# Optimization experiments

Hardware: AMD Instinct MI355X
Metric: run time of the kernel (lower is better)

The kernel has to match this reference:

```python
import jax, jax.numpy as jnp
import numpy as np

V, E, H = 256, 64, 128  # char vocab, char embedding dim, LSTM hidden per direction
N, L = 16384, 24        # number of words, max chars per word


def _lstm_final(embs_t, mask_t, Wih, Whh, bih, bhh):
    """Masked LSTM scan; returns final hidden state [N, H].
    embs_t: [L, N, E] time-major char embeddings
    mask_t: [L, N, 1] float mask (1 = valid char)
    Gate order matches PyTorch: i, f, g, o.
    """
    Nw = embs_t.shape[1]
    h0 = jnp.zeros((Nw, H), embs_t.dtype)
    c0 = jnp.zeros((Nw, H), embs_t.dtype)

    def step(carry, inp):
        h, c = carry
        x, m = inp
        g = x @ Wih.T + bih + h @ Whh.T + bhh  # [N, 4H]
        i, f, gg, o = jnp.split(g, 4, axis=-1)
        i, f, o = jax.nn.sigmoid(i), jax.nn.sigmoid(f), jax.nn.sigmoid(o)
        gg = jnp.tanh(gg)
        c_new = f * c + i * gg
        h_new = o * jnp.tanh(c_new)
        h = jnp.where(m > 0, h_new, h)
        c = jnp.where(m > 0, c_new, c)
        return (h, c), None

    (hT, _), _ = jax.lax.scan(step, (h0, c0), (embs_t, mask_t))
    return hT


def setup_inputs() -> dict:
    key = jax.random.key(0)
    ks = jax.random.split(key, 12)
    s_ih = 1.0 / np.sqrt(H)
    char_indices = jax.random.randint(ks[0], (N, L), 0, V, dtype=jnp.int64)
    lengths = jax.random.randint(ks[1], (N,), 0, L + 1, dtype=jnp.int32)
    emb_table = jax.random.normal(ks[2], (V, E), jnp.float32) * 0.1
    emb_table = emb_table.at[0].set(0.0)  # padding_idx = 0
    def u(k, shape):
        return jax.random.uniform(k, shape, jnp.float32, -s_ih, s_ih)
    return {
        "char_indices": char_indices,
        "lengths": lengths,
        "emb_table": emb_table,
        "Wih_f": u(ks[3], (4 * H, E)),
        "Whh_f": u(ks[4], (4 * H, H)),
        "bih_f": u(ks[5], (4 * H,)),
        "bhh_f": u(ks[6], (4 * H,)),
        "Wih_b": u(ks[7], (4 * H, E)),
        "Whh_b": u(ks[8], (4 * H, H)),
        "bih_b": u(ks[9], (4 * H,)),
        "bhh_b": u(ks[10], (4 * H,)),
    }


def reference(char_indices, lengths, emb_table, Wih_f, Whh_f, bih_f, bhh_f,
              Wih_b, Whh_b, bih_b, bhh_b):
    # mask of valid char positions per word: [N, L]
    pos = jnp.arange(L)[None, :]
    mask = (pos < lengths[:, None]).astype(jnp.float32)
    embs = emb_table[char_indices] * mask[..., None]  # [N, L, E]

    embs_t = jnp.swapaxes(embs, 0, 1)                 # [L, N, E]
    mask_t = jnp.swapaxes(mask, 0, 1)[..., None]      # [L, N, 1]

    # forward direction: final state = state at last valid step
    h_fwd = _lstm_final(embs_t, mask_t, Wih_f, Whh_f, bih_f, bhh_f)
    # backward direction: flip time; leading pad steps are masked (state stays 0),
    # then valid chars are consumed in reverse -> final state = backward h_n
    h_bwd = _lstm_final(embs_t[::-1], mask_t[::-1], Wih_b, Whh_b, bih_b, bhh_b)

    return jnp.concatenate([h_fwd, h_bwd], axis=-1)   # [N, 2H]
```

## Files before the change

kernel.cpp:

```cpp
#include <hip/hip_runtime.h>
#include <math.h>

#define Vv 256
#define Ee 64
#define Hh 128
#define Nn 16384
#define Ll 24
#define G4 512
#define WB 32
#define NTHR 512
#define NGRP (Nn / WB)
#define NTASK (NGRP * 2)

typedef _Float16 half8 __attribute__((ext_vector_type(8)));
typedef float f32x4 __attribute__((ext_vector_type(4)));

#define KS1 (-1.4426950408889634f)

__global__ void prep_sort_kernel(const float* __restrict__ emb,
                                 const float* __restrict__ Wih_f, const float* __restrict__ Whh_f,
                                 const float* __restrict__ bih_f, const float* __restrict__ bhh_f,
                                 const float* __restrict__ Wih_b, const float* __restrict__ Whh_b,
                                 const float* __restrict__ bih_b, const float* __restrict__ bhh_b,
                                 const int* __restrict__ lens,
                                 _Float16* __restrict__ BP, float* __restrict__ XGq,
                                 int* __restrict__ order) {
  const int tid = threadIdx.x;
  if (blockIdx.x == 1024) {
    __shared__ int hcnt[32];
    __shared__ int hcur[32];
    if (tid < 32) hcnt[tid] = 0;
    __syncthreads();
    for (int i = tid; i < Nn; i += 256) atomicAdd(&hcnt[lens[i]], 1);
    __syncthreads();
    if (tid == 0) {
      int s = 0;
      for (int b = 0; b <= Ll; b++) { hcur[b] = s; s += hcnt[b]; }
    }
    __syncthreads();
    for (int i = tid; i < Nn; i += 256) {
      int p = atomicAdd(&hcur[lens[i]], 1);
      order[p] = i;
    }
    return;
  }
  int i = blockIdx.x * 256 + tid;
  if (i < 2 * Vv * G4) {
    int bank = i & 3, u = (i >> 2) & 127, c = (i >> 9) & 255, d = i >> 17;
    int j = bank * 128 + u;
    const float* Wih = d ? Wih_b : Wih_f;
    const float* bih = d ? bih_b : bih_f;
    const float* bhh = d ? bhh_b : bhh_f;
    float acc = bih[j] + bhh[j];
    const float4* e4 = (const float4*)(emb + c * Ee);
    const float4* w4 = (const float4*)(Wih + j * Ee);
#pragma unroll 4
    for (int k = 0; k < Ee / 4; k++) {
      float4 a = e4[k], b = w4[k];
      acc = fmaf(a.x, b.x, acc); acc = fmaf(a.y, b.y, acc);
      acc = fmaf(a.z, b.z, acc); acc = fmaf(a.w, b.w, acc);
    }
    XGq[i] = (bank == 2) ? acc : acc * KS1;
  }
  if (i < 2 * 4 * 4 * 4 * 128 * 8) {
    int e = i & 7, u = (i >> 3) & 127, g2 = (i >> 10) & 3,
        bank = (i >> 12) & 3, kt = (i >> 14) & 3, d = (i >> 16) & 1;
    int j = bank * 128 + u;
    int k = kt * 32 + g2 * 8 + e;
    const float* Whh = d ? Whh_b : Whh_f;
    float w = Whh[j * Hh + k];
    BP[i] = (_Float16)((bank == 2) ? w : w * KS1);
  }
}

#define PADE_TANH(X, NUM, DEN)                                                \
    float X##_2 = (X) * (X);                                                  \
    float NUM = (X) * fmaf(X##_2, fmaf(X##_2, 1.0f, 105.0f), 945.0f);         \
    float DEN = fmaf(X##_2, fmaf(X##_2, 15.0f, 420.0f), 945.0f);              \
    NUM = fminf(fmaxf(NUM, -DEN), DEN);

#define GATES(ACC, CS, HR, MT, WLEN)                                          \
  _Pragma("unroll") for (int r = 0; r < 4; r++) {                             \
    float Av = __builtin_amdgcn_exp2f(ACC[0][r]);                             \
    float Bv = __builtin_amdgcn_exp2f(ACC[1][r]);                             \
    float yg = ACC[2][r];                                                     \
    float Ev = __builtin_amdgcn_exp2f(ACC[3][r]);                             \
    float aA = 1.0f + Av, aB = 1.0f + Bv, aE = 1.0f + Ev;                     \
    PADE_TANH(yg, gn, gd)                                                     \
    float R1 = __builtin_amdgcn_rcpf(aA * aB * gd);                           \
    float cn = fmaf(CS[r] * aA, gd, gn * aB) * R1;                            \
    PADE_TANH(cn, tn, td)                                                     \
    float R2 = __builtin_amdgcn_rcpf(td * aE);                                \
    float hn = tn * R2;                                                       \
    if (t < WLEN[r]) {                                                        \
      CS[r] = cn; HR[r] = hn;                                                 \
      hw[(MT)*16 + qg * 4 + r][u] = (_Float16)hn;                             \
    }                                                                         \
  }

#define LOADX(XV, P0, MT, TT)                                                 \
  _Pragma("unroll") for (int r = 0; r < 4; r++) {                             \
    int pos = P0[r] + sgn * (TT);                                             \
    pos = pos < 0 ? 0 : pos;                                                  \
    int c = idx_s[(MT)*16 + qg * 4 + r][pos];                                 \
    XV[r] = xq[(c << 7) + u];                                                 \
  }

__global__ __launch_bounds__(NTHR, 2) void bilstm_main(
    const int* __restrict__ cidx, const int* __restrict__ lens,
    const _Float16* __restrict__ BP, const float* __restrict__ XGq,
    const int* __restrict__ order, float* __restrict__ out) {
  __shared__ __align__(16) _Float16 hs[2][WB][136];
  __shared__ int idx_s[WB][Ll];
  __shared__ int wid_s[WB];
  __shared__ int len_s[WB];

  const int tid = threadIdx.x;
  const int lane = tid & 63;
  const int wv = tid >> 6;
  const int qg = lane >> 4;
  const int li = lane & 15;
  const int u = (wv << 4) + li;

  const int task = NTASK - 1 - (int)blockIdx.x;
  const int g = task >> 1;
  const int d = task & 1;
  const int sgn = d ? -1 : 1;

  if (tid < WB) { int w = order[g * WB + tid]; wid_s[tid] = w; len_s[tid] = lens[w]; }
  __syncthreads();
  for (int i = tid; i < WB * Ll; i += NTHR) {
    int w = i / Ll, p = i - w * Ll;
    idx_s[w][p] = cidx[(size_t)wid_s[w] * Ll + p];
  }
  for (int i = tid; i < 2 * WB * 136; i += NTHR) ((_Float16*)hs)[i] = (_Float16)0.0f;
  __syncthreads();

  const int maxlen = len_s[WB - 1];

  half8 Bf[4][4];
  {
    const _Float16* BPd = BP + (size_t)d * 65536;
#pragma unroll
    for (int kt = 0; kt < 4; kt++)
#pragma unroll
      for (int bank = 0; bank < 4; bank++)
        Bf[kt][bank] = *(const half8*)(BPd + (size_t)((((kt * 4 + bank) * 4 + qg) * 128 + u) << 3));
  }

  const f32x4* xq = (const f32x4*)(XGq + (size_t)d * (Vv * G4));

  int wlen0[4], wlen1[4], p0a[4], p0b[4];
#pragma unroll
  for (int r = 0; r < 4; r++) {
    wlen0[r] = len_s[qg * 4 + r];
    wlen1[r] = len_s[16 + qg * 4 + r];
    p0a[r] = d ? (wlen0[r] - 1) : 0;
    p0b[r] = d ? (wlen1[r] - 1) : 0;
  }
  float cst0[4], cst1[4], hreg0[4], hreg1[4];
#pragma unroll
  for (int r = 0; r < 4; r++) { cst0[r] = 0.0f; cst1[r] = 0.0f; hreg0[r] = 0.0f; hreg1[r] = 0.0f; }

  f32x4 x4a[4], x4b[4];
  if (maxlen > 0) { LOADX(x4a, p0a, 0, 0); LOADX(x4b, p0b, 1, 0); }

  for (int t = 0; t < maxlen; t++) {
    _Float16 (*hw)[136] = hs[t & 1];
    const _Float16 (*hr)[136] = hs[(t ^ 1) & 1];

    f32x4 acc0[4], acc1[4];
#pragma unroll
    for (int bank = 0; bank < 4; bank++)
#pragma unroll
      for (int r = 0; r < 4; r++) {
        acc0[bank][r] = x4a[r][bank];
        acc1[bank][r] = x4b[r][bank];
      }

    if (t > 0) {
      half8 a0[4], a1[4];
#pragma unroll
      for (int kt = 0; kt < 4; kt++) {
        a0[kt] = *(const half8*)&hr[li][kt * 32 + qg * 8];
        a1[kt] = *(const half8*)&hr[16 + li][kt * 32 + qg * 8];
      }
#pragma unroll
      for (int bank = 0; bank < 4; bank++) {
        f32x4 v0 = acc0[bank], v1 = acc1[bank];
#pragma unroll
        for (int kt = 0; kt < 4; kt++) {
          v0 = __builtin_amdgcn_mfma_f32_16x16x32_f16(a0[kt], Bf[kt][bank], v0, 0, 0, 0);
          v1 = __builtin_amdgcn_mfma_f32_16x16x32_f16(a1[kt], Bf[kt][bank], v1, 0, 0, 0);
        }
        acc0[bank] = v0; acc1[bank] = v1;
      }
    }

    if (t + 1 < maxlen) { LOADX(x4a, p0a, 0, t + 1); LOADX(x4b, p0b, 1, t + 1); }

    GATES(acc0, cst0, hreg0, 0, wlen0);
    GATES(acc1, cst1, hreg1, 1, wlen1);

    __syncthreads();
  }

#pragma unroll
  for (int r = 0; r < 4; r++) {
    out[(size_t)wid_s[qg * 4 + r] * (2 * Hh) + d * Hh + u] = hreg0[r];
    out[(size_t)wid_s[16 + qg * 4 + r] * (2 * Hh) + d * Hh + u] = hreg1[r];
  }
}

extern "C" void kernel_launch(void* const* d_in, const int* in_sizes, int n_in,
                              void* d_out, int out_size, void* d_ws, size_t ws_size,
                              hipStream_t stream) {
  const int* cidx = (const int*)d_in[0];
  const int* lens = (const int*)d_in[1];
  const float* emb = (const float*)d_in[2];
  const float* Wih_f = (const float*)d_in[3];
  const float* Whh_f = (const float*)d_in[4];
  const float* bih_f = (const float*)d_in[5];
  const float* bhh_f = (const float*)d_in[6];
  const float* Wih_b = (const float*)d_in[7];
  const float* Whh_b = (const float*)d_in[8];
  const float* bih_b = (const float*)d_in[9];
  const float* bhh_b = (const float*)d_in[10];
  float* out = (float*)d_out;

  char* base = (char*)d_ws;
  _Float16* BP = (_Float16*)base;
  float* XGq = (float*)(base + 262144);
  int* order = (int*)(base + 262144 + 1048576);

  prep_sort_kernel<<<1025, 256, 0, stream>>>(
      emb, Wih_f, Whh_f, bih_f, bhh_f, Wih_b, Whh_b, bih_b, bhh_b, lens, BP, XGq, order);
  bilstm_main<<<NTASK, NTHR, 0, stream>>>(cidx, lens, BP, XGq, order, out);
}
```

Baseline: 147.6 us.

## Halve words per block to 16, raise occupancy, compute sigmoids via Pade tanh

Each block now handles 16 words instead of 32, which halves per-thread state registers and MFMA work per step. Launch bounds go from 2 to 4 blocks per CU, so more blocks can overlap the serial per-timestep latency. The sigmoid gates are rewritten as 0.5*(1+tanh(x/2)) using the rational Pade tanh with folded reciprocals, removing the exp2 calls. The trade-offs are twice as many blocks and reloads of the recurrent weights, fewer independent MFMA chains per wave to hide latency, and the accuracy of the Pade approximation for the sigmoid gates.

```diff
diff --git a/kernel.cpp b/kernel.cpp
--- a/kernel.cpp
+++ b/kernel.cpp
@@ -7,15 +7,13 @@
 #define Nn 16384
 #define Ll 24
 #define G4 512
-#define WB 32
+#define WB 16
 #define NTHR 512
 #define NGRP (Nn / WB)
 #define NTASK (NGRP * 2)
 
 typedef _Float16 half8 __attribute__((ext_vector_type(8)));
 typedef float f32x4 __attribute__((ext_vector_type(4)));
-
-#define KS1 (-1.4426950408889634f)
 
 __global__ void prep_sort_kernel(const float* __restrict__ emb,
                                  const float* __restrict__ Wih_f, const float* __restrict__ Whh_f,
@@ -60,7 +58,7 @@
       acc = fmaf(a.x, b.x, acc); acc = fmaf(a.y, b.y, acc);
       acc = fmaf(a.z, b.z, acc); acc = fmaf(a.w, b.w, acc);
     }
-    XGq[i] = (bank == 2) ? acc : acc * KS1;
+    XGq[i] = (bank == 2) ? acc : acc * 0.5f;
   }
   if (i < 2 * 4 * 4 * 4 * 128 * 8) {
     int e = i & 7, u = (i >> 3) & 127, g2 = (i >> 10) & 3,
@@ -69,7 +67,7 @@
     int k = kt * 32 + g2 * 8 + e;
     const float* Whh = d ? Whh_b : Whh_f;
     float w = Whh[j * Hh + k];
-    BP[i] = (_Float16)((bank == 2) ? w : w * KS1);
+    BP[i] = (_Float16)((bank == 2) ? w : w * 0.5f);
   }
 }
 
@@ -79,34 +77,38 @@
     float DEN = fmaf(X##_2, fmaf(X##_2, 15.0f, 420.0f), 945.0f);              \
     NUM = fminf(fmaxf(NUM, -DEN), DEN);
 
-#define GATES(ACC, CS, HR, MT, WLEN)                                          \
+#define GATES(ACC, CS, HR, WLEN)                                              \
   _Pragma("unroll") for (int r = 0; r < 4; r++) {                             \
-    float Av = __builtin_amdgcn_exp2f(ACC[0][r]);                             \
-    float Bv = __builtin_amdgcn_exp2f(ACC[1][r]);                             \
+    float xi = ACC[0][r];                                                     \
+    float xf = ACC[1][r];                                                     \
     float yg = ACC[2][r];                                                     \
-    float Ev = __builtin_amdgcn_exp2f(ACC[3][r]);                             \
-    float aA = 1.0f + Av, aB = 1.0f + Bv, aE = 1.0f + Ev;                     \
-    PADE_TANH(yg, gn, gd)                                                     \
-    float R1 = __builtin_amdgcn_rcpf(aA * aB * gd);                           \
-    float cn = fmaf(CS[r] * aA, gd, gn * aB) * R1;                            \
-    PADE_TANH(cn, tn, td)                                                     \
-    float R2 = __builtin_amdgcn_rcpf(td * aE);                                \
-    float hn = tn * R2;                                                       \
+    float xo = ACC[3][r];                                                     \
+    PADE_TANH(xi, ni, di)                                                     \
+    PADE_TANH(xf, nf, df)                                                     \
+    PADE_TANH(yg, ng, dg)                                                     \
+    PADE_TANH(xo, no, od)                                                     \
+    float Pi = di + ni, Pf = df + nf, Po = od + no;                           \
+    float M = di * dg;                                                        \
+    float R1 = __builtin_amdgcn_rcpf((df + df) * M);                          \
+    float cn = fmaf((CS[r] * Pf), M, (Pi * ng) * df) * R1;                    \
+    PADE_TANH(cn, nc, dc)                                                     \
+    float R2 = __builtin_amdgcn_rcpf((od + od) * dc);                         \
+    float hn = (Po * nc) * R2;                                                \
     if (t < WLEN[r]) {                                                        \
       CS[r] = cn; HR[r] = hn;                                                 \
-      hw[(MT)*16 + qg * 4 + r][u] = (_Float16)hn;                             \
+      hw[qg * 4 + r][u] = (_Float16)hn;                                       \
     }                                                                         \
   }
 
-#define LOADX(XV, P0, MT, TT)                                                 \
+#define LOADX(XV, TT)                                                         \
   _Pragma("unroll") for (int r = 0; r < 4; r++) {                             \
-    int pos = P0[r] + sgn * (TT);                                             \
+    int pos = p0a[r] + sgn * (TT);                                            \
     pos = pos < 0 ? 0 : pos;                                                  \
-    int c = idx_s[(MT)*16 + qg * 4 + r][pos];                                 \
+    int c = idx_s[qg * 4 + r][pos];                                           \
     XV[r] = xq[(c << 7) + u];                                                 \
   }
 
-__global__ __launch_bounds__(NTHR, 2) void bilstm_main(
+__global__ __launch_bounds__(NTHR, 4) void bilstm_main(
     const int* __restrict__ cidx, const int* __restrict__ lens,
     const _Float16* __restrict__ BP, const float* __restrict__ XGq,
     const int* __restrict__ order, float* __restrict__ out) {
@@ -150,66 +152,54 @@
 
   const f32x4* xq = (const f32x4*)(XGq + (size_t)d * (Vv * G4));
 
-  int wlen0[4], wlen1[4], p0a[4], p0b[4];
+  int wlen0[4], p0a[4];
 #pragma unroll
   for (int r = 0; r < 4; r++) {
     wlen0[r] = len_s[qg * 4 + r];
-    wlen1[r] = len_s[16 + qg * 4 + r];
     p0a[r] = d ? (wlen0[r] - 1) : 0;
-    p0b[r] = d ? (wlen1[r] - 1) : 0;
-  }
-  float cst0[4], cst1[4], hreg0[4], hreg1[4];
-#pragma unroll
-  for (int r = 0; r < 4; r++) { cst0[r] = 0.0f; cst1[r] = 0.0f; hreg0[r] = 0.0f; hreg1[r] = 0.0f; }
-
-  f32x4 x4a[4], x4b[4];
-  if (maxlen > 0) { LOADX(x4a, p0a, 0, 0); LOADX(x4b, p0b, 1, 0); }
+  }
+  float cst0[4], hreg0[4];
+#pragma unroll
+  for (int r = 0; r < 4; r++) { cst0[r] = 0.0f; hreg0[r] = 0.0f; }
+
+  f32x4 x4a[4];
+  if (maxlen > 0) { LOADX(x4a, 0); }
 
   for (int t = 0; t < maxlen; t++) {
     _Float16 (*hw)[136] = hs[t & 1];
     const _Float16 (*hr)[136] = hs[(t ^ 1) & 1];
 
-    f32x4 acc0[4], acc1[4];
+    f32x4 acc0[4];
 #pragma unroll
     for (int bank = 0; bank < 4; bank++)
 #pragma unroll
-      for (int r = 0; r < 4; r++) {
-        acc0[bank][r] = x4a[r][bank];
-        acc1[bank][r] = x4b[r][bank];
+      for (int r = 0; r < 4; r++) acc0[bank][r] = x4a[r][bank];
+
+    if (t > 0) {
+      half8 a0[4];
+#pragma unroll
+      for (int kt = 0; kt < 4; kt++)
+        a0[kt] = *(const half8*)&hr[li][kt * 32 + qg * 8];
+#pragma unroll
+      for (int bank = 0; bank < 4; bank++) {
+        f32x4 v0 = acc0[bank];
+#pragma unroll
+        for (int kt = 0; kt < 4; kt++)
+          v0 = __builtin_amdgcn_mfma_f32_16x16x32_f16(a0[kt], Bf[kt][bank], v0, 0, 0, 0);
+        acc0[bank] = v0;
       }
-
-    if (t > 0) {
-      half8 a0[4], a1[4];
-#pragma unroll
-      for (int kt = 0; kt < 4; kt++) {
-        a0[kt] = *(const half8*)&hr[li][kt * 32 + qg * 8];
-        a1[kt] = *(const half8*)&hr[16 + li][kt * 32 + qg * 8];
-      }
-#pragma unroll
-      for (int bank = 0; bank < 4; bank++) {
-        f32x4 v0 = acc0[bank], v1 = acc1[bank];
-#pragma unroll
-        for (int kt = 0; kt < 4; kt++) {
-          v0 = __builtin_amdgcn_mfma_f32_16x16x32_f16(a0[kt], Bf[kt][bank], v0, 0, 0, 0);
-          v1 = __builtin_amdgcn_mfma_f32_16x16x32_f16(a1[kt], Bf[kt][bank], v1, 0, 0, 0);
-        }
-        acc0[bank] = v0; acc1[bank] = v1;
-      }
-    }
-
-    if (t + 1 < maxlen) { LOADX(x4a, p0a, 0, t + 1); LOADX(x4b, p0b, 1, t + 1); }
-
-    GATES(acc0, cst0, hreg0, 0, wlen0);
-    GATES(acc1, cst1, hreg1, 1, wlen1);
-
-    __syncthreads();
-  }
-
-#pragma unroll
-  for (int r = 0; r < 4; r++) {
+    }
+
+    if (t + 1 < maxlen) { LOADX(x4a, t + 1); }
+
+    GATES(acc0, cst0, hreg0, wlen0);
+
+    __syncthreads();
+  }
+
+#pragma unroll
+  for (int r = 0; r < 4; r++)
     out[(size_t)wid_s[qg * 4 + r] * (2 * Hh) + d * Hh + u] = hreg0[r];
-    out[(size_t)wid_s[16 + qg * 4 + r] * (2 * Hh) + d * Hh + u] = hreg1[r];
-  }
 }
 
 extern "C" void kernel_launch(void* const* d_in, const int* in_sizes, int n_in,
```

New measurement: 155.5 us. 1.05x slower.

## Cut register pressure to raise occupancy: gather X gates in-loop, bank-major table

Applied to the files above, without the earlier changes.

The precomputed input-gate table is relaid bank-major so each gate bank is read as a separate coalesced scalar load. The prefetch of next-step input gates is removed and the gather happens at the start of each step, directly into the accumulators. MFMA loops are reordered so each A fragment is loaded just before use, and launch bounds go from 2 to 4 blocks per CU. The goal is lower VGPR use so more blocks run at once, at the cost of exposing gather latency on the recurrent critical path.

```diff
diff --git a/kernel.cpp b/kernel.cpp
--- a/kernel.cpp
+++ b/kernel.cpp
@@ -46,7 +46,7 @@
   }
   int i = blockIdx.x * 256 + tid;
   if (i < 2 * Vv * G4) {
-    int bank = i & 3, u = (i >> 2) & 127, c = (i >> 9) & 255, d = i >> 17;
+    int u = i & 127, bank = (i >> 7) & 3, c = (i >> 9) & 255, d = i >> 17;
     int j = bank * 128 + u;
     const float* Wih = d ? Wih_b : Wih_f;
     const float* bih = d ? bih_b : bih_f;
@@ -98,15 +98,19 @@
     }                                                                         \
   }
 
-#define LOADX(XV, P0, MT, TT)                                                 \
+#define GATHER(ACC, P0, MT)                                                   \
   _Pragma("unroll") for (int r = 0; r < 4; r++) {                             \
-    int pos = P0[r] + sgn * (TT);                                             \
+    int pos = P0[r] + sgn * t;                                                \
     pos = pos < 0 ? 0 : pos;                                                  \
     int c = idx_s[(MT)*16 + qg * 4 + r][pos];                                 \
-    XV[r] = xq[(c << 7) + u];                                                 \
-  }
-
-__global__ __launch_bounds__(NTHR, 2) void bilstm_main(
+    const float* xr = xgf + (c << 9) + u;                                     \
+    ACC[0][r] = xr[0];                                                        \
+    ACC[1][r] = xr[128];                                                      \
+    ACC[2][r] = xr[256];                                                      \
+    ACC[3][r] = xr[384];                                                      \
+  }
+
+__global__ __launch_bounds__(NTHR, 4) void bilstm_main(
     const int* __restrict__ cidx, const int* __restrict__ lens,
     const _Float16* __restrict__ BP, const float* __restrict__ XGq,
     const int* __restrict__ order, float* __restrict__ out) {
@@ -133,7 +137,8 @@
     int w = i / Ll, p = i - w * Ll;
     idx_s[w][p] = cidx[(size_t)wid_s[w] * Ll + p];
   }
-  for (int i = tid; i < 2 * WB * 136; i += NTHR) ((_Float16*)hs)[i] = (_Float16)0.0f;
+  for (int i = tid; i < (int)(2 * WB * 136 * sizeof(_Float16) / 16); i += NTHR)
+    ((float4*)hs)[i] = make_float4(0.f, 0.f, 0.f, 0.f);
   __syncthreads();
 
   const int maxlen = len_s[WB - 1];
@@ -148,7 +153,7 @@
         Bf[kt][bank] = *(const half8*)(BPd + (size_t)((((kt * 4 + bank) * 4 + qg) * 128 + u) << 3));
   }
 
-  const f32x4* xq = (const f32x4*)(XGq + (size_t)d * (Vv * G4));
+  const float* xgf = XGq + (size_t)d * (Vv * G4);
 
   int wlen0[4], wlen1[4], p0a[4], p0b[4];
 #pragma unroll
@@ -162,42 +167,30 @@
 #pragma unroll
   for (int r = 0; r < 4; r++) { cst0[r] = 0.0f; cst1[r] = 0.0f; hreg0[r] = 0.0f; hreg1[r] = 0.0f; }
 
-  f32x4 x4a[4], x4b[4];
-  if (maxlen > 0) { LOADX(x4a, p0a, 0, 0); LOADX(x4b, p0b, 1, 0); }
-
   for (int t = 0; t < maxlen; t++) {
     _Float16 (*hw)[136] = hs[t & 1];
     const _Float16 (*hr)[136] = hs[(t ^ 1) & 1];
 
     f32x4 acc0[4], acc1[4];
-#pragma unroll
-    for (int bank = 0; bank < 4; bank++)
-#pragma unroll
-      for (int r = 0; r < 4; r++) {
-        acc0[bank][r] = x4a[r][bank];
-        acc1[bank][r] = x4b[r][bank];
+    GATHER(acc0, p0a, 0)
+    GATHER(acc1, p0b, 1)
+
+    if (t > 0) {
+#pragma unroll
+      for (int kt = 0; kt < 4; kt++) {
+        half8 a0 = *(const half8*)&hr[li][kt * 32 + qg * 8];
+#pragma unroll
+        for (int bank = 0; bank < 4; bank++)
+          acc0[bank] = __builtin_amdgcn_mfma_f32_16x16x32_f16(a0, Bf[kt][bank], acc0[bank], 0, 0, 0);
       }
-
-    if (t > 0) {
-      half8 a0[4], a1[4];
 #pragma unroll
       for (int kt = 0; kt < 4; kt++) {
-        a0[kt] = *(const half8*)&hr[li][kt * 32 + qg * 8];
-        a1[kt] = *(const half8*)&hr[16 + li][kt * 32 + qg * 8];
+        half8 a1 = *(const half8*)&hr[16 + li][kt * 32 + qg * 8];
+#pragma unroll
+        for (int bank = 0; bank < 4; bank++)
+          acc1[bank] = __builtin_amdgcn_mfma_f32_16x16x32_f16(a1, Bf[kt][bank], acc1[bank], 0, 0, 0);
       }
-#pragma unroll
-      for (int bank = 0; bank < 4; bank++) {
-        f32x4 v0 = acc0[bank], v1 = acc1[bank];
-#pragma unroll
-        for (int kt = 0; kt < 4; kt++) {
-          v0 = __builtin_amdgcn_mfma_f32_16x16x32_f16(a0[kt], Bf[kt][bank], v0, 0, 0, 0);
-          v1 = __builtin_amdgcn_mfma_f32_16x16x32_f16(a1[kt], Bf[kt][bank], v1, 0, 0, 0);
-        }
-        acc0[bank] = v0; acc1[bank] = v1;
-      }
-    }
-
-    if (t + 1 < maxlen) { LOADX(x4a, p0a, 0, t + 1); LOADX(x4b, p0b, 1, t + 1); }
+    }
 
     GATES(acc0, cst0, hreg0, 0, wlen0);
     GATES(acc1, cst1, hreg1, 1, wlen1);
```

New measurement: 412.4 us. 2.79x slower.
